# Optimization experiments

Measured on AMD Instinct MI355X. Metric: run time of the kernel, lower is better.

Reference implementation:

```python
import jax, jax.numpy as jnp
import numpy as np

B, S, D, H = 4, 2048, 1024, 16
DEPTH = D // H
NEG = 1e10


def setup_inputs() -> dict:
    key = jax.random.key(0)
    ks = jax.random.split(key, 11)
    sc = 0.02
    return {
        "q": jax.random.normal(ks[0], (B, S, D), jnp.float32),
        "v": jax.random.normal(ks[1], (B, S, D), jnp.float32),
        "k": jax.random.normal(ks[2], (B, S, D), jnp.float32),
        "Wq": jax.random.normal(ks[3], (D, D), jnp.float32) * sc,
        "bq": jnp.zeros((D,), jnp.float32),
        "Wk": jax.random.normal(ks[4], (D, D), jnp.float32) * sc,
        "bk": jnp.zeros((D,), jnp.float32),
        "Wv": jax.random.normal(ks[5], (D, D), jnp.float32) * sc,
        "bv": jnp.zeros((D,), jnp.float32),
        "Wo": jax.random.normal(ks[6], (D, D), jnp.float32) * sc,
        "bo": jnp.zeros((D,), jnp.float32),
        "mask": 1,
    }


def _split_heads(x):
    # [B, S, D] -> [B, H, S, depth]
    b, s, _ = x.shape
    return x.reshape(b, s, H, DEPTH).transpose(0, 2, 1, 3)


def reference(q, v, k, Wq, bq, Wk, bk, Wv, bv, Wo, bo, mask):
    qh = _split_heads(q @ Wq + bq)
    kh = _split_heads(k @ Wk + bk)
    vh = _split_heads(v @ Wv + bv)

    scale = 1.0 / jnp.sqrt(jnp.asarray(DEPTH, jnp.float32))
    # [B, H, Sq, Sk]
    logits = jnp.einsum("bhqd,bhkd->bhqk", qh, kh) * scale

    if mask:
        nd, ns = logits.shape[-2], logits.shape[-1]
        i = jnp.arange(nd)[:, None]
        j = jnp.arange(ns)[None, :]
        b = (i >= j - ns + nd).astype(logits.dtype)  # lower triangle from lower-right
        logits = logits * b - NEG * (1.0 - b)

    attn = jax.nn.softmax(logits, axis=-1)
    out = jnp.einsum("bhqk,bhkd->bhqd", attn, vh)  # [B, H, Sq, depth]
    out = out.transpose(0, 2, 1, 3).reshape(q.shape[0], -1, D)  # concat heads
    return out @ Wo + bo
```

## Files before the change

### kernel.cpp

```cpp
#include <hip/hip_runtime.h>
#include <hip/hip_bf16.h>
#include <cstdint>
#include <cstddef>

#define S_LEN 2048
#define D_MODEL 1024
#define N_HEADS 16
#define DEPTH 64
#define BATCH 4

#define GLOBAL_AS __attribute__((address_space(1)))
#define LDS_AS __attribute__((address_space(3)))

typedef __attribute__((ext_vector_type(4))) float f32x4;
typedef __attribute__((ext_vector_type(8))) short bf16x8;
typedef __attribute__((ext_vector_type(4))) unsigned short us4;
typedef __attribute__((ext_vector_type(8))) unsigned short us8;

__device__ __forceinline__ unsigned short f2bf(float f) {
  unsigned int u = __builtin_bit_cast(unsigned int, f);
  u += 0x7FFFu + ((u >> 16) & 1u);
  return (unsigned short)(u >> 16);
}

__device__ __forceinline__ unsigned short f2bf_hw(float f) {
  return __builtin_bit_cast(unsigned short, __float2bfloat16(f));
}

__global__ __launch_bounds__(256) void transpose_cast(const float* __restrict__ W,
                                                      unsigned short* __restrict__ Wt,
                                                      int N, float scale) {
  __shared__ float tile[32][33];
  int bx = blockIdx.x * 32;
  int by = blockIdx.y * 32;
  int tx = threadIdx.x, ty = threadIdx.y;
#pragma unroll
  for (int i = 0; i < 4; ++i)
    tile[ty + i * 8][tx] = W[(size_t)(by + ty + i * 8) * N + bx + tx];
  __syncthreads();
#pragma unroll
  for (int i = 0; i < 4; ++i)
    Wt[(size_t)(bx + ty + i * 8) * N + by + tx] = f2bf(tile[tx][ty + i * 8] * scale);
}

__global__ __launch_bounds__(256) void transpose_v(const unsigned short* __restrict__ Vp,
                                                   unsigned short* __restrict__ Vt) {
  __shared__ unsigned short tile[64][72];
  int tid = threadIdx.x;
  int sb = blockIdx.x;
  int bh = blockIdx.y;
  int b = bh >> 4, h = bh & 15;
  int s0 = sb * 64;
#pragma unroll
  for (int rep = 0; rep < 2; ++rep) {
    int idx = rep * 256 + tid;
    int r = idx >> 3, c8 = idx & 7;
    us8 v = *(const us8*)(Vp + (size_t)(b * S_LEN + s0 + r) * D_MODEL + h * DEPTH + c8 * 8);
#pragma unroll
    for (int e = 0; e < 8; ++e) tile[c8 * 8 + e][r] = v[e];
  }
  __syncthreads();
#pragma unroll
  for (int rep = 0; rep < 2; ++rep) {
    int idx = rep * 256 + tid;
    int d = idx >> 3, c8 = idx & 7;
    us8 v = *(const us8*)&tile[d][c8 * 8];
    *(us8*)(Vt + ((size_t)(bh * DEPTH + d)) * S_LEN + s0 + c8 * 8) = v;
  }
}

struct GemmSlice {
  const void* A;
  const unsigned short* Bt;
  const float* bias;
  void* C;
  float bscale;
};
struct GemmArgs {
  GemmSlice s[3];
};

template <bool A_IS_F32, bool OUT_F32>
__global__ __launch_bounds__(256) void gemm_bt(GemmArgs args, int M, int N, int K) {
  constexpr int ASTR = A_IS_F32 ? 72 : 64;
  __shared__ unsigned short a_lds[128 * ASTR];
  __shared__ unsigned short b_lds[128 * 64];

  int slice = blockIdx.y >> 3;
  int nj = blockIdx.y & 7;
  const GemmSlice& g = args.s[slice];
  const float* Af = (const float*)g.A;
  const unsigned short* Ah = (const unsigned short*)g.A;
  const unsigned short* Bt = g.Bt;

  int tid = threadIdx.x;
  int wave = tid >> 6, lane = tid & 63;
  int l15 = lane & 15, lg = lane >> 4;
  int wm = wave >> 1, wn = wave & 1;

  int row0 = blockIdx.x * 128;
  int col0 = nj * 128;

  f32x4 acc[4][4] = {};
  f32x4 av[8];

  int ar = tid >> 4, ac4 = tid & 15;

  auto loadA = [&](int k0) {
#pragma unroll
    for (int rep = 0; rep < 8; ++rep)
      av[rep] = *(const f32x4*)(Af + (size_t)(row0 + rep * 16 + ar) * K + k0 + ac4 * 4);
  };
  auto writeA = [&]() {
#pragma unroll
    for (int rep = 0; rep < 8; ++rep) {
      us4 h = {f2bf_hw(av[rep][0]), f2bf_hw(av[rep][1]),
               f2bf_hw(av[rep][2]), f2bf_hw(av[rep][3])};
      *(us4*)&a_lds[(rep * 16 + ar) * 72 + ac4 * 4] = h;
    }
  };
  auto issueA = [&](int k0) {
#pragma unroll
    for (int rep = 0; rep < 4; ++rep) {
      int chunk = (wave * 4 + rep) * 64 + lane;
      int row = chunk >> 3;
      int c8 = (chunk & 7) ^ (row & 7);
      __builtin_amdgcn_global_load_lds(
          (const GLOBAL_AS void*)(Ah + (size_t)(row0 + row) * K + k0 + c8 * 8),
          (LDS_AS void*)(&a_lds[chunk * 8]), 16, 0, 0);
    }
  };
  auto issueB = [&](int k0) {
#pragma unroll
    for (int rep = 0; rep < 4; ++rep) {
      int chunk = (wave * 4 + rep) * 64 + lane;
      int row = chunk >> 3;
      int c8 = (chunk & 7) ^ (row & 7);
      __builtin_amdgcn_global_load_lds(
          (const GLOBAL_AS void*)(Bt + (size_t)(col0 + row) * K + k0 + c8 * 8),
          (LDS_AS void*)(&b_lds[chunk * 8]), 16, 0, 0);
    }
  };
  auto compute = [&]() {
#pragma unroll
    for (int kk = 0; kk < 2; ++kk) {
      bf16x8 af[4], bfr[4];
#pragma unroll
      for (int ii = 0; ii < 4; ++ii) {
        int row = wm * 64 + ii * 16 + l15;
        if constexpr (A_IS_F32)
          af[ii] = *(const bf16x8*)&a_lds[row * 72 + kk * 32 + lg * 8];
        else
          af[ii] = *(const bf16x8*)&a_lds[row * 64 + (((kk * 4 + lg) ^ (l15 & 7)) * 8)];
      }
#pragma unroll
      for (int jj = 0; jj < 4; ++jj) {
        int row = wn * 64 + jj * 16 + l15;
        bfr[jj] = *(const bf16x8*)&b_lds[row * 64 + (((kk * 4 + lg) ^ (l15 & 7)) * 8)];
      }
#pragma unroll
      for (int ii = 0; ii < 4; ++ii)
#pragma unroll
        for (int jj = 0; jj < 4; ++jj)
          acc[ii][jj] = __builtin_amdgcn_mfma_f32_16x16x32_bf16(af[ii], bfr[jj], acc[ii][jj], 0, 0, 0);
    }
  };

  int nk = K >> 6;
  if constexpr (A_IS_F32) loadA(0);

  for (int ki = 0; ki < nk; ++ki) {
    __syncthreads();
    issueB(ki * 64);
    if constexpr (A_IS_F32)
      writeA();
    else
      issueA(ki * 64);
    __syncthreads();
    if constexpr (A_IS_F32) {
      if (ki + 1 < nk) loadA((ki + 1) * 64);
    }
    compute();
  }

#pragma unroll
  for (int ii = 0; ii < 4; ++ii) {
#pragma unroll
    for (int jj = 0; jj < 4; ++jj) {
      int col = col0 + wn * 64 + jj * 16 + l15;
      float bv = g.bias[col] * g.bscale;
#pragma unroll
      for (int r = 0; r < 4; ++r) {
        int row = row0 + wm * 64 + ii * 16 + lg * 4 + r;
        float v = acc[ii][jj][r] + bv;
        if constexpr (OUT_F32)
          ((float*)g.C)[(size_t)row * N + col] = v;
        else
          ((unsigned short*)g.C)[(size_t)row * N + col] = f2bf(v);
      }
    }
  }
}

__global__ __launch_bounds__(512, 8) void attn_kernel(const unsigned short* __restrict__ Qp,
                                                      const unsigned short* __restrict__ Kp,
                                                      const unsigned short* __restrict__ Vt,
                                                      unsigned short* __restrict__ Op) {
  __shared__ unsigned short k_lds[64][76];
  __shared__ unsigned short vt_lds[64][76];
  __shared__ unsigned short p_lds[8][16][76];

  int tid = threadIdx.x;
  int w = tid >> 6, lane = tid & 63;
  int l15 = lane & 15, lg = lane >> 4;

  int bid = blockIdx.x;
  int swz = (bid & 7) * 64 + (bid >> 3);
  int pairIdx = swz & 7;
  int bh = swz >> 3;
  int b = bh >> 4, h = bh & 15;

  const unsigned short* Kbase = Kp + (size_t)b * S_LEN * D_MODEL + h * DEPTH;
  const unsigned short* Vbase = Vt + (size_t)bh * DEPTH * S_LEN;

  bool stageV = (tid >= 256);
  int st = tid & 255;
  int r = st >> 2, cb = (st & 3) * 16;
  const unsigned short* srow = stageV ? (Vbase + (size_t)r * S_LEN + cb)
                                      : (Kbase + (size_t)r * D_MODEL + cb);
  const size_t sstep = stageV ? 64 : (size_t)64 * D_MODEL;

  bf16x8 ones;
#pragma unroll
  for (int e = 0; e < 8; ++e) ones[e] = (short)0x3F80;

  for (int half = 0; half < 2; ++half) {
    int t = (half == 0) ? pairIdx : (15 - pairIdx);
    int q0 = t * 128;
    int nkv = 2 * t + 2;
    int q0w = q0 + w * 16;

    const unsigned short* qp =
        Qp + ((size_t)(b * S_LEN + q0 + w * 16 + l15)) * D_MODEL + h * DEPTH;
    bf16x8 qf0 = *(const bf16x8*)(qp + lg * 8);
    bf16x8 qf1 = *(const bf16x8*)(qp + 32 + lg * 8);

    f32x4 acc_l = (f32x4){0.f, 0.f, 0.f, 0.f};
    f32x4 acc_o[4];
#pragma unroll
    for (int dd = 0; dd < 4; ++dd) acc_o[dd] = (f32x4){0.f, 0.f, 0.f, 0.f};

    const unsigned short* sptr = srow;
    us8 s0 = *(const us8*)sptr;
    us8 s1 = *(const us8*)(sptr + 8);
    sptr += sstep;

    for (int kb = 0; kb < nkv; ++kb) {
      int k0 = kb * 64;
      __syncthreads();
      if (stageV) {
        *(us8*)&vt_lds[r][cb] = s0;
        *(us8*)&vt_lds[r][cb + 8] = s1;
      } else {
        *(us8*)&k_lds[r][cb] = s0;
        *(us8*)&k_lds[r][cb + 8] = s1;
      }
      __syncthreads();
      bool more = (kb + 1) < nkv;
      if (more) {
        s0 = *(const us8*)sptr;
        s1 = *(const us8*)(sptr + 8);
        sptr += sstep;
      }

      bool full_masked = (k0 > q0w + 15);
      if (!full_masked) {
        f32x4 s[4];
#pragma unroll
        for (int nf = 0; nf < 4; ++nf) s[nf] = (f32x4){0.f, 0.f, 0.f, 0.f};
        __builtin_amdgcn_s_setprio(1);
#pragma unroll
        for (int nf = 0; nf < 4; ++nf) {
          bf16x8 kf0 = *(const bf16x8*)&k_lds[nf * 16 + l15][lg * 8];
          bf16x8 kf1 = *(const bf16x8*)&k_lds[nf * 16 + l15][32 + lg * 8];
          s[nf] = __builtin_amdgcn_mfma_f32_16x16x32_bf16(qf0, kf0, s[nf], 0, 0, 0);
          s[nf] = __builtin_amdgcn_mfma_f32_16x16x32_bf16(qf1, kf1, s[nf], 0, 0, 0);
        }
        __builtin_amdgcn_s_setprio(0);

        bool diag = (k0 + 63 > q0w);
        if (diag) {
#pragma unroll
          for (int nf = 0; nf < 4; ++nf)
#pragma unroll
            for (int rr = 0; rr < 4; ++rr) {
              int qrow = q0w + lg * 4 + rr;
              int kcol = k0 + nf * 16 + l15;
              float x = (kcol > qrow) ? -1e10f : s[nf][rr];
              float p = __builtin_amdgcn_exp2f(x);
              p_lds[w][lg * 4 + rr][nf * 16 + l15] =
                  (unsigned short)(__builtin_bit_cast(unsigned int, p) >> 16);
            }
        } else {
#pragma unroll
          for (int nf = 0; nf < 4; ++nf)
#pragma unroll
            for (int rr = 0; rr < 4; ++rr) {
              float p = __builtin_amdgcn_exp2f(s[nf][rr]);
              p_lds[w][lg * 4 + rr][nf * 16 + l15] =
                  (unsigned short)(__builtin_bit_cast(unsigned int, p) >> 16);
            }
        }

        __builtin_amdgcn_s_setprio(1);
#pragma unroll
        for (int kk = 0; kk < 2; ++kk) {
          bf16x8 pf = *(const bf16x8*)&p_lds[w][l15][kk * 32 + lg * 8];
          acc_l = __builtin_amdgcn_mfma_f32_16x16x32_bf16(pf, ones, acc_l, 0, 0, 0);
#pragma unroll
          for (int dd = 0; dd < 4; ++dd) {
            bf16x8 vf = *(const bf16x8*)&vt_lds[dd * 16 + l15][kk * 32 + lg * 8];
            acc_o[dd] = __builtin_amdgcn_mfma_f32_16x16x32_bf16(pf, vf, acc_o[dd], 0, 0, 0);
          }
        }
        __builtin_amdgcn_s_setprio(0);
      }
    }

#pragma unroll
    for (int rr = 0; rr < 4; ++rr) {
      float inv = 1.0f / acc_l[rr];
      int qrow = q0 + w * 16 + lg * 4 + rr;
      unsigned short* op = Op + ((size_t)(b * S_LEN + qrow)) * D_MODEL + h * DEPTH;
#pragma unroll
      for (int dd = 0; dd < 4; ++dd)
        op[dd * 16 + l15] = f2bf(acc_o[dd][rr] * inv);
    }
  }
}

extern "C" void kernel_launch(void* const* d_in, const int* in_sizes, int n_in,
                              void* d_out, int out_size, void* d_ws, size_t ws_size,
                              hipStream_t stream) {
  const float* q  = (const float*)d_in[0];
  const float* v  = (const float*)d_in[1];
  const float* k  = (const float*)d_in[2];
  const float* Wq = (const float*)d_in[3];
  const float* bq = (const float*)d_in[4];
  const float* Wk = (const float*)d_in[5];
  const float* bk = (const float*)d_in[6];
  const float* Wv = (const float*)d_in[7];
  const float* bv = (const float*)d_in[8];
  const float* Wo = (const float*)d_in[9];
  const float* bo = (const float*)d_in[10];

  char* ws = (char*)d_ws;
  const size_t WSZ = (size_t)D_MODEL * D_MODEL * 2;
  const size_t XSZ = (size_t)BATCH * S_LEN * D_MODEL * 2;
  unsigned short* Wqt = (unsigned short*)(ws);
  unsigned short* Wkt = (unsigned short*)(ws + WSZ);
  unsigned short* Wvt = (unsigned short*)(ws + 2 * WSZ);
  unsigned short* Wot = (unsigned short*)(ws + 3 * WSZ);
  unsigned short* Qp  = (unsigned short*)(ws + 4 * WSZ);
  unsigned short* Kp  = (unsigned short*)(ws + 4 * WSZ + XSZ);
  unsigned short* Vp  = (unsigned short*)(ws + 4 * WSZ + 2 * XSZ);
  unsigned short* Vtp = (unsigned short*)(ws + 4 * WSZ + 3 * XSZ);
  unsigned short* AO  = Vp;

  const float SCL = 0.125f * 1.4426950408889634f;
  const int M = BATCH * S_LEN;

  dim3 tb(32, 8);
  dim3 tg(D_MODEL / 32, D_MODEL / 32);
  hipLaunchKernelGGL(transpose_cast, tg, tb, 0, stream, Wq, Wqt, D_MODEL, SCL);
  hipLaunchKernelGGL(transpose_cast, tg, tb, 0, stream, Wk, Wkt, D_MODEL, 1.0f);
  hipLaunchKernelGGL(transpose_cast, tg, tb, 0, stream, Wv, Wvt, D_MODEL, 1.0f);
  hipLaunchKernelGGL(transpose_cast, tg, tb, 0, stream, Wo, Wot, D_MODEL, 1.0f);

  GemmArgs qkv{};
  qkv.s[0] = GemmSlice{(const void*)q, Wqt, bq, (void*)Qp, SCL};
  qkv.s[1] = GemmSlice{(const void*)k, Wkt, bk, (void*)Kp, 1.0f};
  qkv.s[2] = GemmSlice{(const void*)v, Wvt, bv, (void*)Vp, 1.0f};
  hipLaunchKernelGGL((gemm_bt<true, false>), dim3(M / 128, 24), dim3(256), 0, stream,
                     qkv, M, D_MODEL, D_MODEL);

  hipLaunchKernelGGL(transpose_v, dim3(S_LEN / 64, BATCH * N_HEADS), dim3(256), 0, stream,
                     Vp, Vtp);

  hipLaunchKernelGGL(attn_kernel, dim3(512), dim3(512), 0, stream, Qp, Kp, Vtp, AO);

  GemmArgs ao{};
  ao.s[0] = GemmSlice{(const void*)AO, Wot, bo, d_out, 1.0f};
  hipLaunchKernelGGL((gemm_bt<false, true>), dim3(M / 128, 8), dim3(256), 0, stream,
                     ao, M, D_MODEL, D_MODEL);
}
```

Measured before the change: 222.8 us.

## Register-prefetch B tiles in GEMM and merge four weight transposes into one launch

The GEMM now loads the next B tile into registers during the current tile's compute and writes it to padded LDS, replacing direct global-to-LDS loads with an XOR swizzle. This is meant to hide B-load latency behind the MFMA work. The four weight transpose-cast launches become one launch with a z dimension, which removes launch overhead. The cost is more register pressure from the prefetch buffer, plus a larger padded LDS footprint for B that may reduce occupancy.

```diff
diff --git a/kernel.cpp b/kernel.cpp
--- a/kernel.cpp
+++ b/kernel.cpp
@@ -27,10 +27,18 @@
   return __builtin_bit_cast(unsigned short, __float2bfloat16(f));
 }
 
-__global__ __launch_bounds__(256) void transpose_cast(const float* __restrict__ W,
-                                                      unsigned short* __restrict__ Wt,
-                                                      int N, float scale) {
+struct TCArgs {
+  const float* W[4];
+  unsigned short* Wt[4];
+  float scale[4];
+};
+
+__global__ __launch_bounds__(256) void transpose_cast4(TCArgs a, int N) {
   __shared__ float tile[32][33];
+  int z = blockIdx.z;
+  const float* W = a.W[z];
+  unsigned short* Wt = a.Wt[z];
+  float scale = a.scale[z];
   int bx = blockIdx.x * 32;
   int by = blockIdx.y * 32;
   int tx = threadIdx.x, ty = threadIdx.y;
@@ -84,7 +92,7 @@
 __global__ __launch_bounds__(256) void gemm_bt(GemmArgs args, int M, int N, int K) {
   constexpr int ASTR = A_IS_F32 ? 72 : 64;
   __shared__ unsigned short a_lds[128 * ASTR];
-  __shared__ unsigned short b_lds[128 * 64];
+  __shared__ unsigned short b_lds[128 * 72];
 
   int slice = blockIdx.y >> 3;
   int nj = blockIdx.y & 7;
@@ -103,8 +111,10 @@
 
   f32x4 acc[4][4] = {};
   f32x4 av[8];
+  us8 bv[4];
 
   int ar = tid >> 4, ac4 = tid & 15;
+  int br = tid >> 3, bc8 = tid & 7;
 
   auto loadA = [&](int k0) {
 #pragma unroll
@@ -118,6 +128,16 @@
                f2bf_hw(av[rep][2]), f2bf_hw(av[rep][3])};
       *(us4*)&a_lds[(rep * 16 + ar) * 72 + ac4 * 4] = h;
     }
+  };
+  auto loadB = [&](int k0) {
+#pragma unroll
+    for (int rep = 0; rep < 4; ++rep)
+      bv[rep] = *(const us8*)(Bt + (size_t)(col0 + rep * 32 + br) * K + k0 + bc8 * 8);
+  };
+  auto writeB = [&]() {
+#pragma unroll
+    for (int rep = 0; rep < 4; ++rep)
+      *(us8*)&b_lds[(rep * 32 + br) * 72 + bc8 * 8] = bv[rep];
   };
   auto issueA = [&](int k0) {
 #pragma unroll
@@ -130,17 +150,6 @@
           (LDS_AS void*)(&a_lds[chunk * 8]), 16, 0, 0);
     }
   };
-  auto issueB = [&](int k0) {
-#pragma unroll
-    for (int rep = 0; rep < 4; ++rep) {
-      int chunk = (wave * 4 + rep) * 64 + lane;
-      int row = chunk >> 3;
-      int c8 = (chunk & 7) ^ (row & 7);
-      __builtin_amdgcn_global_load_lds(
-          (const GLOBAL_AS void*)(Bt + (size_t)(col0 + row) * K + k0 + c8 * 8),
-          (LDS_AS void*)(&b_lds[chunk * 8]), 16, 0, 0);
-    }
-  };
   auto compute = [&]() {
 #pragma unroll
     for (int kk = 0; kk < 2; ++kk) {
@@ -156,7 +165,7 @@
 #pragma unroll
       for (int jj = 0; jj < 4; ++jj) {
         int row = wn * 64 + jj * 16 + l15;
-        bfr[jj] = *(const bf16x8*)&b_lds[row * 64 + (((kk * 4 + lg) ^ (l15 & 7)) * 8)];
+        bfr[jj] = *(const bf16x8*)&b_lds[row * 72 + kk * 32 + lg * 8];
       }
 #pragma unroll
       for (int ii = 0; ii < 4; ++ii)
@@ -167,18 +176,20 @@
   };
 
   int nk = K >> 6;
+  loadB(0);
   if constexpr (A_IS_F32) loadA(0);
 
   for (int ki = 0; ki < nk; ++ki) {
     __syncthreads();
-    issueB(ki * 64);
+    writeB();
     if constexpr (A_IS_F32)
       writeA();
     else
       issueA(ki * 64);
     __syncthreads();
-    if constexpr (A_IS_F32) {
-      if (ki + 1 < nk) loadA((ki + 1) * 64);
+    if (ki + 1 < nk) {
+      loadB((ki + 1) * 64);
+      if constexpr (A_IS_F32) loadA((ki + 1) * 64);
     }
     compute();
   }
@@ -188,11 +199,11 @@
 #pragma unroll
     for (int jj = 0; jj < 4; ++jj) {
       int col = col0 + wn * 64 + jj * 16 + l15;
-      float bv = g.bias[col] * g.bscale;
+      float bv2 = g.bias[col] * g.bscale;
 #pragma unroll
       for (int r = 0; r < 4; ++r) {
         int row = row0 + wm * 64 + ii * 16 + lg * 4 + r;
-        float v = acc[ii][jj][r] + bv;
+        float v = acc[ii][jj][r] + bv2;
         if constexpr (OUT_F32)
           ((float*)g.C)[(size_t)row * N + col] = v;
         else
@@ -370,12 +381,13 @@
   const float SCL = 0.125f * 1.4426950408889634f;
   const int M = BATCH * S_LEN;
 
-  dim3 tb(32, 8);
-  dim3 tg(D_MODEL / 32, D_MODEL / 32);
-  hipLaunchKernelGGL(transpose_cast, tg, tb, 0, stream, Wq, Wqt, D_MODEL, SCL);
-  hipLaunchKernelGGL(transpose_cast, tg, tb, 0, stream, Wk, Wkt, D_MODEL, 1.0f);
-  hipLaunchKernelGGL(transpose_cast, tg, tb, 0, stream, Wv, Wvt, D_MODEL, 1.0f);
-  hipLaunchKernelGGL(transpose_cast, tg, tb, 0, stream, Wo, Wot, D_MODEL, 1.0f);
+  TCArgs tc{};
+  tc.W[0] = Wq;  tc.Wt[0] = Wqt;  tc.scale[0] = SCL;
+  tc.W[1] = Wk;  tc.Wt[1] = Wkt;  tc.scale[1] = 1.0f;
+  tc.W[2] = Wv;  tc.Wt[2] = Wvt;  tc.scale[2] = 1.0f;
+  tc.W[3] = Wo;  tc.Wt[3] = Wot;  tc.scale[3] = 1.0f;
+  hipLaunchKernelGGL(transpose_cast4, dim3(D_MODEL / 32, D_MODEL / 32, 4), dim3(32, 8),
+                     0, stream, tc, D_MODEL);
 
   GemmArgs qkv{};
   qkv.s[0] = GemmSlice{(const void*)q, Wqt, bq, (void*)Qp, SCL};
```

New measurement: 211.3 us. 5.1% less time.
